# Kernel tuning notes

Hardware: AMD Instinct MI355X
Metric: run time of the kernel (lower is better)

## Reference

```python
import jax, jax.numpy as jnp
import numpy as np

HIDDEN = 2048
NUM_HEADS = 16
HEAD_DIM = 128
WINDOW = 256
BATCH = 2
SEQ = 2048
ROPE_BASE = 10000.0


def apply_rope(t):
    # t: [b, h, s, d]; half-split (rotate-half) rotary embedding
    d = t.shape[-1]
    s = t.shape[-2]
    inv_freq = 1.0 / (ROPE_BASE ** (jnp.arange(0, d, 2, dtype=jnp.float32) / d))  # [d/2]
    freqs = jnp.arange(s, dtype=jnp.float32)[:, None] * inv_freq[None, :]          # [s, d/2]
    cos, sin = jnp.cos(freqs), jnp.sin(freqs)
    t1, t2 = t[..., : d // 2], t[..., d // 2 :]
    return jnp.concatenate([t1 * cos - t2 * sin, t1 * sin + t2 * cos], axis=-1)


def setup_inputs() -> dict:
    key = jax.random.key(0)
    ks = jax.random.split(key, 10)
    dm = HEAD_DIM * NUM_HEADS
    lin_std = 1.0 / np.sqrt(HIDDEN)
    out_std = 1.0 / np.sqrt(dm)
    return {
        "x": jax.random.normal(ks[0], (BATCH, SEQ, HIDDEN), dtype=jnp.float32),
        "W_Q": jax.random.uniform(ks[1], (HIDDEN, dm), jnp.float32, -lin_std, lin_std),
        "b_Q": jax.random.uniform(ks[2], (dm,), jnp.float32, -lin_std, lin_std),
        "W_K": jax.random.uniform(ks[3], (HIDDEN, dm), jnp.float32, -lin_std, lin_std),
        "b_K": jax.random.uniform(ks[4], (dm,), jnp.float32, -lin_std, lin_std),
        "W_V": jax.random.uniform(ks[5], (HIDDEN, dm), jnp.float32, -lin_std, lin_std),
        "b_V": jax.random.uniform(ks[6], (dm,), jnp.float32, -lin_std, lin_std),
        "W_O": jax.random.uniform(ks[7], (dm, HIDDEN), jnp.float32, -out_std, out_std),
        "b_O": jax.random.uniform(ks[8], (HIDDEN,), jnp.float32, -out_std, out_std),
        "key_weights": jax.random.normal(ks[9], (NUM_HEADS,), dtype=jnp.float32),
    }


def reference(x, W_Q, b_Q, W_K, b_K, W_V, b_V, W_O, b_O, key_weights):
    b, s, _ = x.shape
    scale = HEAD_DIM ** -0.5

    def split_heads(t):  # [b, s, h*d] -> [b, h, s, d]
        return t.reshape(b, s, NUM_HEADS, HEAD_DIM).transpose(0, 2, 1, 3)

    q = split_heads(x @ W_Q + b_Q)
    k = split_heads(x @ W_K + b_K)
    v = split_heads(x @ W_V + b_V)

    q = apply_rope(q)
    k = apply_rope(k)

    # num_kv_heads == num_heads here, so group_size == 1: plain per-head attention
    scores = jnp.einsum("bhqd,bhkd->bhqk", q, k) * scale
    scores = scores * key_weights[None, :, None, None]

    # sliding-window causal mask: allow 0 <= i - j <= WINDOW
    i = jnp.arange(s)[:, None]
    j = jnp.arange(s)[None, :]
    allowed = (j <= i) & (j >= i - WINDOW)
    scores = jnp.where(allowed[None, None], scores, -jnp.inf)

    attn = jax.nn.softmax(scores, axis=-1)
    out = jnp.einsum("bhqk,bhkd->bhqd", attn, v)  # [b, h, s, d]
    out = out.transpose(0, 2, 1, 3).reshape(b, s, NUM_HEADS * HEAD_DIM)
    return out @ W_O + b_O
```

## Files before the change

### kernel.cpp

```cpp
#include <hip/hip_runtime.h>
#include <cstdint>

#define SEQn   2048
#define NHn    16
#define HDn    128
#define DMn    2048
#define HIDn   2048
#define BATCHn 2
#define WINn   256
#define MROWS  (BATCHn*SEQn)
#define WELEMS ((size_t)HIDn * DMn)

typedef short s16x8 __attribute__((ext_vector_type(8)));
typedef float f32x4 __attribute__((ext_vector_type(4)));

__device__ __forceinline__ float bf2f(ushort x) {
    union { uint u; float f; } v; v.u = ((uint)x) << 16; return v.f;
}
__device__ __forceinline__ ushort f2bf(float f) {
    union { float f; uint u; } v; v.f = f;
    uint u = v.u;
    return (ushort)((u + 0x7FFFu + ((u >> 16) & 1u)) >> 16);
}

#define GLOAD_LDS16(g, l) __builtin_amdgcn_global_load_lds(                   \
    (const __attribute__((address_space(1))) unsigned int*)(g),               \
    (__attribute__((address_space(3))) unsigned int*)(l), 16, 0, 0)

__global__ __launch_bounds__(256)
void transpose_all_kernel(const float* __restrict__ WQ, const float* __restrict__ WK,
                          const float* __restrict__ WV, const float* __restrict__ WO,
                          ushort* __restrict__ WT,
                          const float* __restrict__ x, ushort* __restrict__ xb)
{
    const int tid = threadIdx.y * 32 + threadIdx.x;
    if (blockIdx.z == 4) {
        const int bid = blockIdx.y * 64 + blockIdx.x;
        const size_t base = ((size_t)bid * 256 + tid) * 8;
        const float4 a0 = *reinterpret_cast<const float4*>(x + base);
        const float4 a1 = *reinterpret_cast<const float4*>(x + base + 4);
        ushort4 o0, o1;
        o0.x = f2bf(a0.x); o0.y = f2bf(a0.y); o0.z = f2bf(a0.z); o0.w = f2bf(a0.w);
        o1.x = f2bf(a1.x); o1.y = f2bf(a1.y); o1.z = f2bf(a1.z); o1.w = f2bf(a1.w);
        *reinterpret_cast<ushort4*>(xb + base)     = o0;
        *reinterpret_cast<ushort4*>(xb + base + 4) = o1;
        return;
    }
    __shared__ ushort t[32][33];
    const float* src = (blockIdx.z == 0) ? WQ : (blockIdx.z == 1) ? WK
                     : (blockIdx.z == 2) ? WV : WO;
    ushort* dst = WT + (size_t)blockIdx.z * WELEMS;
    const int tx = threadIdx.x, ty = threadIdx.y;
    const int n  = blockIdx.x * 32 + tx;
    const int k0 = blockIdx.y * 32;
    #pragma unroll
    for (int r = ty; r < 32; r += 8)
        t[r][tx] = f2bf(src[(size_t)(k0 + r) * 2048 + n]);
    __syncthreads();
    const int k  = k0 + tx;
    const int nb = blockIdx.x * 32;
    #pragma unroll
    for (int r = ty; r < 32; r += 8)
        dst[(size_t)(nb + r) * 2048 + k] = t[tx][r];
}

__global__ __launch_bounds__(256)
void transpose_cvt_kernel(const float* __restrict__ src, ushort* __restrict__ dst)
{
    __shared__ ushort t[32][33];
    const int tx = threadIdx.x, ty = threadIdx.y;
    const int n  = blockIdx.x * 32 + tx;
    const int k0 = blockIdx.y * 32;
    #pragma unroll
    for (int r = ty; r < 32; r += 8)
        t[r][tx] = f2bf(src[(size_t)(k0 + r) * 2048 + n]);
    __syncthreads();
    const int k  = k0 + tx;
    const int nb = blockIdx.x * 32;
    #pragma unroll
    for (int r = ty; r < 32; r += 8)
        dst[(size_t)(nb + r) * 2048 + k] = t[tx][r];
}

template<int ABF16>
__global__ __launch_bounds__(256)
void gemm_qkv_kernel(const void* __restrict__ Araw, const ushort* __restrict__ WT,
                     const float* __restrict__ bQ, const float* __restrict__ bK,
                     const float* __restrict__ bV,
                     ushort* __restrict__ Qb, ushort* __restrict__ Kb,
                     ushort* __restrict__ Vt)
{
    __shared__ __align__(16) ushort smem[128 * 136];
    ushort* As = smem;
    ushort* Bs = smem + 128 * 64;
    const int tid = threadIdx.x;
    const int m0  = blockIdx.y * 128;
    const int n0g = blockIdx.x * 128;
    const int sel = n0g >> 11;
    const int n0  = n0g & 2047;
    const ushort* BT  = WT + (size_t)sel * WELEMS;
    const float* bias = (sel == 0) ? bQ : (sel == 1) ? bK : bV;
    const int w  = tid >> 6;
    const int l  = tid & 63;
    const int wy = w >> 1, wx = w & 1;
    const int q  = l >> 4, lm = l & 15;
    const int sw = lm & 7;

    f32x4 acc[4][4];
    #pragma unroll
    for (int i = 0; i < 4; ++i)
        #pragma unroll
        for (int j = 0; j < 4; ++j) acc[i][j] = (f32x4)0.0f;

    for (int kt = 0; kt < HIDn; kt += 64) {
        if (ABF16) {
            #pragma unroll
            for (int it = 0; it < 4; ++it) {
                const int v = it * 256 + tid;
                const int r = v >> 3;
                const int cs = ((v & 7) ^ (r & 7)) << 3;
                const ushort* gA = (const ushort*)Araw + (size_t)(m0 + r) * HIDn + kt + cs;
                const ushort* gB = BT + (size_t)(n0 + r) * HIDn + kt + cs;
                GLOAD_LDS16(gA, As + (it * 256 + w * 64) * 8);
                GLOAD_LDS16(gB, Bs + (it * 256 + w * 64) * 8);
            }
        } else {
            #pragma unroll
            for (int it = 0; it < 4; ++it) {
                const int v = it * 256 + tid;
                const int r = v >> 3;
                const int c = (v & 7) << 3;
                const float* Af = (const float*)Araw + (size_t)(m0 + r) * HIDn + kt + c;
                const float4 a0 = *reinterpret_cast<const float4*>(Af);
                const float4 a1 = *reinterpret_cast<const float4*>(Af + 4);
                ushort* d = &As[(size_t)(v ^ (r & 7)) * 8];
                d[0] = f2bf(a0.x); d[1] = f2bf(a0.y); d[2] = f2bf(a0.z); d[3] = f2bf(a0.w);
                d[4] = f2bf(a1.x); d[5] = f2bf(a1.y); d[6] = f2bf(a1.z); d[7] = f2bf(a1.w);
                const int cs = ((v & 7) ^ (r & 7)) << 3;
                const ushort* gB = BT + (size_t)(n0 + r) * HIDn + kt + cs;
                GLOAD_LDS16(gB, Bs + (it * 256 + w * 64) * 8);
            }
        }
        __syncthreads();
        #pragma unroll
        for (int ks = 0; ks < 2; ++ks) {
            s16x8 af[4], bfv[4];
            #pragma unroll
            for (int im = 0; im < 4; ++im) {
                const int arow = wy * 64 + im * 16 + lm;
                af[im] = *reinterpret_cast<const s16x8*>(
                    &As[arow * 64 + (((ks * 4 + q) ^ sw) << 3)]);
            }
            #pragma unroll
            for (int in = 0; in < 4; ++in) {
                const int brow = wx * 64 + in * 16 + lm;
                bfv[in] = *reinterpret_cast<const s16x8*>(
                    &Bs[brow * 64 + (((ks * 4 + q) ^ sw) << 3)]);
            }
            #pragma unroll
            for (int im = 0; im < 4; ++im)
                #pragma unroll
                for (int in = 0; in < 4; ++in)
                    acc[im][in] = __builtin_amdgcn_mfma_f32_16x16x32_bf16(af[im], bfv[in], acc[im][in], 0, 0, 0);
        }
        __syncthreads();
    }

    if (sel == 2) {
        #pragma unroll
        for (int in = 0; in < 4; ++in) {
            const int gcol = n0 + wx * 64 + in * 16 + lm;
            const float bv = bias[gcol];
            #pragma unroll
            for (int im = 0; im < 4; ++im) {
                const int grow0 = m0 + wy * 64 + im * 16 + q * 4;
                #pragma unroll
                for (int r = 0; r < 4; ++r) {
                    const float val = acc[im][in][r] + bv;
                    const int grow = grow0 + r;
                    const int bb = grow >> 11, s = grow & (SEQn - 1);
                    const int hh = gcol >> 7,  d = gcol & (HDn - 1);
                    Vt[(((size_t)(bb * NHn + hh)) * HDn + d) * SEQn + s] = f2bf(val);
                }
            }
        }
    } else {
        ushort* ctile = smem;
        #pragma unroll
        for (int in = 0; in < 4; ++in) {
            const int col = wx * 64 + in * 16 + lm;
            const float bv = bias[n0 + col];
            #pragma unroll
            for (int im = 0; im < 4; ++im) {
                const int row0 = wy * 64 + im * 16 + q * 4;
                #pragma unroll
                for (int r = 0; r < 4; ++r)
                    ctile[(row0 + r) * 136 + col] = f2bf(acc[im][in][r] + bv);
            }
        }
        __syncthreads();
        ushort* dst = (sel == 0) ? Qb : Kb;
        const int d = tid & 63;
        const float invf = exp2f(-(float)d * 0.20762050593046f);
        for (int r = tid >> 6; r < 128; r += 4) {
            const int s = (m0 + r) & (SEQn - 1);
            const float ang = (float)s * invf;
            float sn, cs;
            __sincosf(ang, &sn, &cs);
            const float t1 = bf2f(ctile[r * 136 + d]);
            const float t2 = bf2f(ctile[r * 136 + 64 + d]);
            const size_t base = (size_t)(m0 + r) * DMn + n0 + d;
            dst[base]      = f2bf(t1 * cs - t2 * sn);
            dst[base + 64] = f2bf(t1 * sn + t2 * cs);
        }
    }
}

__global__ __launch_bounds__(256)
void gemm_out_kernel(const ushort* __restrict__ A, const ushort* __restrict__ BT,
                     const float* __restrict__ bias, float* __restrict__ C)
{
    __shared__ __align__(16) ushort As[64 * 64];
    __shared__ __align__(16) ushort Bs[128 * 64];
    const int tid = threadIdx.x;
    const int m0 = blockIdx.y * 64;
    const int n0 = blockIdx.x * 128;
    const int w  = tid >> 6;
    const int l  = tid & 63;
    const int wy = w >> 1, wx = w & 1;
    const int q  = l >> 4, lm = l & 15;
    const int sw = lm & 7;

    f32x4 acc[2][4];
    #pragma unroll
    for (int i = 0; i < 2; ++i)
        #pragma unroll
        for (int j = 0; j < 4; ++j) acc[i][j] = (f32x4)0.0f;

    for (int kt = 0; kt < DMn; kt += 64) {
        #pragma unroll
        for (int it = 0; it < 2; ++it) {
            const int v = it * 256 + tid;
            const int r = v >> 3;
            const int cs = ((v & 7) ^ (r & 7)) << 3;
            const ushort* gA = A + (size_t)(m0 + r) * DMn + kt + cs;
            GLOAD_LDS16(gA, As + (it * 256 + w * 64) * 8);
        }
        #pragma unroll
        for (int it = 0; it < 4; ++it) {
            const int v = it * 256 + tid;
            const int r = v >> 3;
            const int cs = ((v & 7) ^ (r & 7)) << 3;
            const ushort* gB = BT + (size_t)(n0 + r) * DMn + kt + cs;
            GLOAD_LDS16(gB, Bs + (it * 256 + w * 64) * 8);
        }
        __syncthreads();
        #pragma unroll
        for (int ks = 0; ks < 2; ++ks) {
            s16x8 af[2], bfv[4];
            #pragma unroll
            for (int im = 0; im < 2; ++im) {
                const int arow = wy * 32 + im * 16 + lm;
                af[im] = *reinterpret_cast<const s16x8*>(
                    &As[arow * 64 + (((ks * 4 + q) ^ sw) << 3)]);
            }
            #pragma unroll
            for (int in = 0; in < 4; ++in) {
                const int brow = wx * 64 + in * 16 + lm;
                bfv[in] = *reinterpret_cast<const s16x8*>(
                    &Bs[brow * 64 + (((ks * 4 + q) ^ sw) << 3)]);
            }
            #pragma unroll
            for (int im = 0; im < 2; ++im)
                #pragma unroll
                for (int in = 0; in < 4; ++in)
                    acc[im][in] = __builtin_amdgcn_mfma_f32_16x16x32_bf16(af[im], bfv[in], acc[im][in], 0, 0, 0);
        }
        __syncthreads();
    }
    #pragma unroll
    for (int in = 0; in < 4; ++in) {
        const int gcol = n0 + wx * 64 + in * 16 + lm;
        const float bv = bias[gcol];
        #pragma unroll
        for (int im = 0; im < 2; ++im) {
            const int grow0 = m0 + wy * 32 + im * 16 + q * 4;
            #pragma unroll
            for (int r = 0; r < 4; ++r)
                C[(size_t)(grow0 + r) * HIDn + gcol] = acc[im][in][r] + bv;
        }
    }
}

__global__ __launch_bounds__(256)
void attn_mfma_kernel(const ushort* Q, const ushort* __restrict__ K,
                      const ushort* __restrict__ Vt, const float* __restrict__ kw,
                      ushort* AO)
{
    __shared__ ushort plds[4][16 * 40];
    const int w  = threadIdx.x >> 6;
    const int l  = threadIdx.x & 63;
    const int q  = l >> 4, lm = l & 15;
    const int gw = blockIdx.x * 4 + w;
    const int qt = gw & 127;
    const int h  = (gw >> 7) & (NHn - 1);
    const int b  = gw >> 11;
    const int q0 = qt * 16;
    const float f = kw[h] * 0.08838834764831845f;

    s16x8 qf[4];
    const size_t qbase = ((size_t)(b * SEQn + q0 + lm)) * DMn + h * HDn;
    #pragma unroll
    for (int ks = 0; ks < 4; ++ks)
        qf[ks] = *reinterpret_cast<const s16x8*>(Q + qbase + ks * 32 + q * 8);

    f32x4 O[8];
    #pragma unroll
    for (int nt = 0; nt < 8; ++nt) O[nt] = (f32x4)0.0f;
    float m[4]    = {-1e30f, -1e30f, -1e30f, -1e30f};
    float lsum[4] = {0.f, 0.f, 0.f, 0.f};

    const int lo = q0 - WINn;
    const int c0 = lo > 0 ? (lo & ~31) : 0;
    const int nch = (q0 + 16 - c0 + 31) >> 5;

    const size_t kbh = ((size_t)(b * SEQn)) * DMn + h * HDn;
    const size_t vbh = ((size_t)(b * NHn + h)) * HDn * SEQn;

    for (int c = 0; c < nch; ++c) {
        const int kc = c0 + c * 32;
        s16x8 vf[8];
        #pragma unroll
        for (int nt = 0; nt < 8; ++nt)
            vf[nt] = *reinterpret_cast<const s16x8*>(
                Vt + vbh + (size_t)(nt * 16 + lm) * SEQn + kc + q * 8);
        f32x4 S[2];
        #pragma unroll
        for (int t = 0; t < 2; ++t) {
            f32x4 acc = (f32x4)0.0f;
            const size_t krow = kbh + (size_t)(kc + t * 16 + lm) * DMn;
            #pragma unroll
            for (int ks = 0; ks < 4; ++ks) {
                const s16x8 kf = *reinterpret_cast<const s16x8*>(K + krow + ks * 32 + q * 8);
                acc = __builtin_amdgcn_mfma_f32_16x16x32_bf16(qf[ks], kf, acc, 0, 0, 0);
            }
            S[t] = acc;
        }
        const int j0 = kc + lm, j1 = kc + 16 + lm;
        #pragma unroll
        for (int r = 0; r < 4; ++r) {
            const int i = q0 + q * 4 + r;
            float v0 = S[0][r] * f;
            float v1 = S[1][r] * f;
            if (j0 > i || j0 < i - WINn) v0 = -1e30f;
            if (j1 > i || j1 < i - WINn) v1 = -1e30f;
            float mx = fmaxf(v0, v1);
            #pragma unroll
            for (int off = 8; off > 0; off >>= 1)
                mx = fmaxf(mx, __shfl_xor(mx, off));
            const float mn = fmaxf(m[r], mx);
            const float alpha = __expf(m[r] - mn);
            m[r] = mn;
            const ushort h0 = f2bf(__expf(v0 - mn));
            const ushort h1 = f2bf(__expf(v1 - mn));
            plds[w][(q * 4 + r) * 40 + lm]      = h0;
            plds[w][(q * 4 + r) * 40 + 16 + lm] = h1;
            float ps = bf2f(h0) + bf2f(h1);
            #pragma unroll
            for (int off = 8; off > 0; off >>= 1)
                ps += __shfl_xor(ps, off);
            lsum[r] = lsum[r] * alpha + ps;
            #pragma unroll
            for (int nt = 0; nt < 8; ++nt) O[nt][r] *= alpha;
        }
        const s16x8 pf = *reinterpret_cast<const s16x8*>(&plds[w][lm * 40 + q * 8]);
        #pragma unroll
        for (int nt = 0; nt < 8; ++nt)
            O[nt] = __builtin_amdgcn_mfma_f32_16x16x32_bf16(pf, vf[nt], O[nt], 0, 0, 0);
    }
    #pragma unroll
    for (int r = 0; r < 4; ++r) {
        const float inv = 1.0f / lsum[r];
        const size_t orow = ((size_t)(b * SEQn + q0 + q * 4 + r)) * DMn + h * HDn;
        #pragma unroll
        for (int nt = 0; nt < 8; ++nt)
            AO[orow + nt * 16 + lm] = f2bf(O[nt][r] * inv);
    }
}

extern "C" void kernel_launch(void* const* d_in, const int* in_sizes, int n_in,
                              void* d_out, int out_size, void* d_ws, size_t ws_size,
                              hipStream_t stream)
{
    (void)in_sizes; (void)n_in; (void)out_size;
    const float* x  = (const float*)d_in[0];
    const float* WQ = (const float*)d_in[1];
    const float* bQ = (const float*)d_in[2];
    const float* WK = (const float*)d_in[3];
    const float* bK = (const float*)d_in[4];
    const float* WV = (const float*)d_in[5];
    const float* bV = (const float*)d_in[6];
    const float* WO = (const float*)d_in[7];
    const float* bO = (const float*)d_in[8];
    const float* kw = (const float*)d_in[9];
    float* out = (float*)d_out;

    char* ws = (char*)d_ws;
    const size_t AELEMS = (size_t)MROWS * DMn;
    ushort* Qb = (ushort*)ws;
    ushort* Kb = (ushort*)(ws + AELEMS * 2);
    ushort* Vt = (ushort*)(ws + AELEMS * 4);
    ushort* WT = (ushort*)(ws + AELEMS * 6);
    const size_t FULL = AELEMS * 6 + WELEMS * 8 + AELEMS * 2;
    const bool have_full = ws_size >= FULL;
    ushort* xb = (ushort*)(ws + AELEMS * 6 + WELEMS * 8);

    const dim3 tblk(32, 8);

    if (have_full) {
        transpose_all_kernel<<<dim3(64, 64, 5), tblk, 0, stream>>>(WQ, WK, WV, WO, WT, x, xb);
        gemm_qkv_kernel<1><<<dim3(3 * DMn / 128, MROWS / 128), 256, 0, stream>>>(
            xb, WT, bQ, bK, bV, Qb, Kb, Vt);
        attn_mfma_kernel<<<dim3(BATCHn * NHn * (SEQn / 16) / 4), 256, 0, stream>>>(Qb, Kb, Vt, kw, Qb);
        gemm_out_kernel<<<dim3(HIDn / 128, MROWS / 64), 256, 0, stream>>>(
            Qb, WT + 3 * WELEMS, bO, out);
    } else {
        transpose_all_kernel<<<dim3(64, 64, 3), tblk, 0, stream>>>(WQ, WK, WV, WO, WT, x, xb);
        gemm_qkv_kernel<0><<<dim3(3 * DMn / 128, MROWS / 128), 256, 0, stream>>>(
            x, WT, bQ, bK, bV, Qb, Kb, Vt);
        attn_mfma_kernel<<<dim3(BATCHn * NHn * (SEQn / 16) / 4), 256, 0, stream>>>(Qb, Kb, Vt, kw, Qb);
        transpose_cvt_kernel<<<dim3(64, 64), tblk, 0, stream>>>(WO, WT);
        gemm_out_kernel<<<dim3(HIDn / 128, MROWS / 64), 256, 0, stream>>>(Qb, WT, bO, out);
    }
}
```

Measured before the change: 403.6 us.

## Double-buffer GEMM LDS tiles, stage V transpose via LDS, add MFMA priority hints

Both GEMM kernels now use two LDS slots. The next K-tile's global-to-LDS loads are issued before computing the current tile, with explicit vmcnt waits and raw barriers, so memory latency can overlap MFMA work. The V projection epilogue writes its transposed tile to LDS first and then stores it coalesced to Vt, replacing scattered 2-byte stores. s_setprio raises wave priority around the MFMA blocks in the GEMMs and attention, and the attention K fragments are loaded before their MFMAs. The doubled LDS footprint may lower occupancy, and the hand-written waitcnt counts must match the number of loads issued per stage.

New measurement: 374.5 us. 7.2% less time.

```diff
diff --git a/kernel.cpp b/kernel.cpp
--- a/kernel.cpp
+++ b/kernel.cpp
@@ -26,6 +26,9 @@
 #define GLOAD_LDS16(g, l) __builtin_amdgcn_global_load_lds(                   \
     (const __attribute__((address_space(1))) unsigned int*)(g),               \
     (__attribute__((address_space(3))) unsigned int*)(l), 16, 0, 0)
+
+#define FENCE() do { asm volatile("" ::: "memory");                           \
+                     __builtin_amdgcn_sched_barrier(0); } while (0)
 
 __global__ __launch_bounds__(256)
 void transpose_all_kernel(const float* __restrict__ WQ, const float* __restrict__ WK,
@@ -90,9 +93,7 @@
                      ushort* __restrict__ Qb, ushort* __restrict__ Kb,
                      ushort* __restrict__ Vt)
 {
-    __shared__ __align__(16) ushort smem[128 * 136];
-    ushort* As = smem;
-    ushort* Bs = smem + 128 * 64;
+    __shared__ __align__(16) ushort smem[32768];
     const int tid = threadIdx.x;
     const int m0  = blockIdx.y * 128;
     const int n0g = blockIdx.x * 128;
@@ -112,7 +113,9 @@
         #pragma unroll
         for (int j = 0; j < 4; ++j) acc[i][j] = (f32x4)0.0f;
 
-    for (int kt = 0; kt < HIDn; kt += 64) {
+    auto stage = [&](int slot, int kt) {
+        ushort* AsS = smem + slot * 16384;
+        ushort* BsS = AsS + 8192;
         if (ABF16) {
             #pragma unroll
             for (int it = 0; it < 4; ++it) {
@@ -121,8 +124,8 @@
                 const int cs = ((v & 7) ^ (r & 7)) << 3;
                 const ushort* gA = (const ushort*)Araw + (size_t)(m0 + r) * HIDn + kt + cs;
                 const ushort* gB = BT + (size_t)(n0 + r) * HIDn + kt + cs;
-                GLOAD_LDS16(gA, As + (it * 256 + w * 64) * 8);
-                GLOAD_LDS16(gB, Bs + (it * 256 + w * 64) * 8);
+                GLOAD_LDS16(gA, AsS + (it * 256 + w * 64) * 8);
+                GLOAD_LDS16(gB, BsS + (it * 256 + w * 64) * 8);
             }
         } else {
             #pragma unroll
@@ -133,15 +136,19 @@
                 const float* Af = (const float*)Araw + (size_t)(m0 + r) * HIDn + kt + c;
                 const float4 a0 = *reinterpret_cast<const float4*>(Af);
                 const float4 a1 = *reinterpret_cast<const float4*>(Af + 4);
-                ushort* d = &As[(size_t)(v ^ (r & 7)) * 8];
+                ushort* d = &AsS[(size_t)(v ^ (r & 7)) * 8];
                 d[0] = f2bf(a0.x); d[1] = f2bf(a0.y); d[2] = f2bf(a0.z); d[3] = f2bf(a0.w);
                 d[4] = f2bf(a1.x); d[5] = f2bf(a1.y); d[6] = f2bf(a1.z); d[7] = f2bf(a1.w);
                 const int cs = ((v & 7) ^ (r & 7)) << 3;
                 const ushort* gB = BT + (size_t)(n0 + r) * HIDn + kt + cs;
-                GLOAD_LDS16(gB, Bs + (it * 256 + w * 64) * 8);
-            }
-        }
-        __syncthreads();
+                GLOAD_LDS16(gB, BsS + (it * 256 + w * 64) * 8);
+            }
+        }
+    };
+
+    auto compute = [&](int slot) {
+        const ushort* AsS = smem + slot * 16384;
+        const ushort* BsS = AsS + 8192;
         #pragma unroll
         for (int ks = 0; ks < 2; ++ks) {
             s16x8 af[4], bfv[4];
@@ -149,40 +156,74 @@
             for (int im = 0; im < 4; ++im) {
                 const int arow = wy * 64 + im * 16 + lm;
                 af[im] = *reinterpret_cast<const s16x8*>(
-                    &As[arow * 64 + (((ks * 4 + q) ^ sw) << 3)]);
+                    &AsS[arow * 64 + (((ks * 4 + q) ^ sw) << 3)]);
             }
             #pragma unroll
             for (int in = 0; in < 4; ++in) {
                 const int brow = wx * 64 + in * 16 + lm;
                 bfv[in] = *reinterpret_cast<const s16x8*>(
-                    &Bs[brow * 64 + (((ks * 4 + q) ^ sw) << 3)]);
-            }
+                    &BsS[brow * 64 + (((ks * 4 + q) ^ sw) << 3)]);
+            }
+            __builtin_amdgcn_s_setprio(1);
             #pragma unroll
             for (int im = 0; im < 4; ++im)
                 #pragma unroll
                 for (int in = 0; in < 4; ++in)
                     acc[im][in] = __builtin_amdgcn_mfma_f32_16x16x32_bf16(af[im], bfv[in], acc[im][in], 0, 0, 0);
+            __builtin_amdgcn_s_setprio(0);
+        }
+    };
+
+    const int NT = HIDn / 64;
+    stage(0, 0);
+    int cur = 0;
+    for (int t = 0; t < NT - 1; ++t) {
+        stage(cur ^ 1, (t + 1) * 64);
+        if (ABF16) asm volatile("s_waitcnt vmcnt(8)" ::: "memory");
+        else       asm volatile("s_waitcnt vmcnt(4)" ::: "memory");
+        __builtin_amdgcn_s_barrier();
+        FENCE();
+        compute(cur);
+        FENCE();
+        if (!ABF16) asm volatile("s_waitcnt lgkmcnt(0)" ::: "memory");
+        __builtin_amdgcn_s_barrier();
+        FENCE();
+        cur ^= 1;
+    }
+    asm volatile("s_waitcnt vmcnt(0)" ::: "memory");
+    __builtin_amdgcn_s_barrier();
+    FENCE();
+    compute(cur);
+    __syncthreads();
+
+    if (sel == 2) {
+        ushort* ctile = smem;
+        #pragma unroll
+        for (int in = 0; in < 4; ++in) {
+            const int col = wx * 64 + in * 16 + lm;
+            const float bv = bias[n0 + col];
+            #pragma unroll
+            for (int im = 0; im < 4; ++im) {
+                const int row0 = wy * 64 + im * 16 + q * 4;
+                #pragma unroll
+                for (int r = 0; r < 4; ++r)
+                    ctile[col * 136 + row0 + r] = f2bf(acc[im][in][r] + bv);
+            }
         }
         __syncthreads();
-    }
-
-    if (sel == 2) {
-        #pragma unroll
-        for (int in = 0; in < 4; ++in) {
-            const int gcol = n0 + wx * 64 + in * 16 + lm;
-            const float bv = bias[gcol];
-            #pragma unroll
-            for (int im = 0; im < 4; ++im) {
-                const int grow0 = m0 + wy * 64 + im * 16 + q * 4;
-                #pragma unroll
-                for (int r = 0; r < 4; ++r) {
-                    const float val = acc[im][in][r] + bv;
-                    const int grow = grow0 + r;
-                    const int bb = grow >> 11, s = grow & (SEQn - 1);
-                    const int hh = gcol >> 7,  d = gcol & (HDn - 1);
-                    Vt[(((size_t)(bb * NHn + hh)) * HDn + d) * SEQn + s] = f2bf(val);
-                }
-            }
+        const int hh = n0 >> 7;
+        const int bb = m0 >> 11;
+        const int s0 = m0 & (SEQn - 1);
+        const int st = (tid & 15) * 8;
+        const int d0 = tid >> 4;
+        #pragma unroll
+        for (int db = 0; db < 8; ++db) {
+            const int d = d0 + db * 16;
+            const ushort4 v0 = *reinterpret_cast<const ushort4*>(&ctile[d * 136 + st]);
+            const ushort4 v1 = *reinterpret_cast<const ushort4*>(&ctile[d * 136 + st + 4]);
+            ushort* dstp = Vt + (((size_t)(bb * NHn + hh)) * HDn + d) * SEQn + s0 + st;
+            *reinterpret_cast<ushort4*>(dstp)     = v0;
+            *reinterpret_cast<ushort4*>(dstp + 4) = v1;
         }
     } else {
         ushort* ctile = smem;
@@ -220,8 +261,7 @@
 void gemm_out_kernel(const ushort* __restrict__ A, const ushort* __restrict__ BT,
                      const float* __restrict__ bias, float* __restrict__ C)
 {
-    __shared__ __align__(16) ushort As[64 * 64];
-    __shared__ __align__(16) ushort Bs[128 * 64];
+    __shared__ __align__(16) ushort smem[24576];
     const int tid = threadIdx.x;
     const int m0 = blockIdx.y * 64;
     const int n0 = blockIdx.x * 128;
@@ -237,24 +277,30 @@
         #pragma unroll
         for (int j = 0; j < 4; ++j) acc[i][j] = (f32x4)0.0f;
 
-    for (int kt = 0; kt < DMn; kt += 64) {
+    auto stage = [&](int slot, int kt) {
+        ushort* AsS = smem + slot * 12288;
+        ushort* BsS = AsS + 4096;
         #pragma unroll
         for (int it = 0; it < 2; ++it) {
             const int v = it * 256 + tid;
             const int r = v >> 3;
             const int cs = ((v & 7) ^ (r & 7)) << 3;
-            const ushort* gA = A + (size_t)(m0 + r) * DMn + kt + cs;
-            GLOAD_LDS16(gA, As + (it * 256 + w * 64) * 8);
+            GLOAD_LDS16(A + (size_t)(m0 + r) * DMn + kt + cs,
+                        AsS + (it * 256 + w * 64) * 8);
         }
         #pragma unroll
         for (int it = 0; it < 4; ++it) {
             const int v = it * 256 + tid;
             const int r = v >> 3;
             const int cs = ((v & 7) ^ (r & 7)) << 3;
-            const ushort* gB = BT + (size_t)(n0 + r) * DMn + kt + cs;
-            GLOAD_LDS16(gB, Bs + (it * 256 + w * 64) * 8);
-        }
-        __syncthreads();
+            GLOAD_LDS16(BT + (size_t)(n0 + r) * DMn + kt + cs,
+                        BsS + (it * 256 + w * 64) * 8);
+        }
+    };
+
+    auto compute = [&](int slot) {
+        const ushort* AsS = smem + slot * 12288;
+        const ushort* BsS = AsS + 4096;
         #pragma unroll
         for (int ks = 0; ks < 2; ++ks) {
             s16x8 af[2], bfv[4];
@@ -262,22 +308,43 @@
             for (int im = 0; im < 2; ++im) {
                 const int arow = wy * 32 + im * 16 + lm;
                 af[im] = *reinterpret_cast<const s16x8*>(
-                    &As[arow * 64 + (((ks * 4 + q) ^ sw) << 3)]);
+                    &AsS[arow * 64 + (((ks * 4 + q) ^ sw) << 3)]);
             }
             #pragma unroll
             for (int in = 0; in < 4; ++in) {
                 const int brow = wx * 64 + in * 16 + lm;
                 bfv[in] = *reinterpret_cast<const s16x8*>(
-                    &Bs[brow * 64 + (((ks * 4 + q) ^ sw) << 3)]);
-            }
+                    &BsS[brow * 64 + (((ks * 4 + q) ^ sw) << 3)]);
+            }
+            __builtin_amdgcn_s_setprio(1);
             #pragma unroll
             for (int im = 0; im < 2; ++im)
                 #pragma unroll
                 for (int in = 0; in < 4; ++in)
                     acc[im][in] = __builtin_amdgcn_mfma_f32_16x16x32_bf16(af[im], bfv[in], acc[im][in], 0, 0, 0);
-        }
-        __syncthreads();
-    }
+            __builtin_amdgcn_s_setprio(0);
+        }
+    };
+
+    const int NT = DMn / 64;
+    stage(0, 0);
+    int cur = 0;
+    for (int t = 0; t < NT - 1; ++t) {
+        stage(cur ^ 1, (t + 1) * 64);
+        asm volatile("s_waitcnt vmcnt(6)" ::: "memory");
+        __builtin_amdgcn_s_barrier();
+        FENCE();
+        compute(cur);
+        FENCE();
+        __builtin_amdgcn_s_barrier();
+        FENCE();
+        cur ^= 1;
+    }
+    asm volatile("s_waitcnt vmcnt(0)" ::: "memory");
+    __builtin_amdgcn_s_barrier();
+    FENCE();
+    compute(cur);
+
     #pragma unroll
     for (int in = 0; in < 4; ++in) {
         const int gcol = n0 + wx * 64 + in * 16 + lm;
@@ -339,11 +406,15 @@
         for (int t = 0; t < 2; ++t) {
             f32x4 acc = (f32x4)0.0f;
             const size_t krow = kbh + (size_t)(kc + t * 16 + lm) * DMn;
-            #pragma unroll
-            for (int ks = 0; ks < 4; ++ks) {
-                const s16x8 kf = *reinterpret_cast<const s16x8*>(K + krow + ks * 32 + q * 8);
-                acc = __builtin_amdgcn_mfma_f32_16x16x32_bf16(qf[ks], kf, acc, 0, 0, 0);
-            }
+            s16x8 kf[4];
+            #pragma unroll
+            for (int ks = 0; ks < 4; ++ks)
+                kf[ks] = *reinterpret_cast<const s16x8*>(K + krow + ks * 32 + q * 8);
+            __builtin_amdgcn_s_setprio(1);
+            #pragma unroll
+            for (int ks = 0; ks < 4; ++ks)
+                acc = __builtin_amdgcn_mfma_f32_16x16x32_bf16(qf[ks], kf[ks], acc, 0, 0, 0);
+            __builtin_amdgcn_s_setprio(0);
             S[t] = acc;
         }
         const int j0 = kc + lm, j1 = kc + 16 + lm;
@@ -374,9 +445,11 @@
             for (int nt = 0; nt < 8; ++nt) O[nt][r] *= alpha;
         }
         const s16x8 pf = *reinterpret_cast<const s16x8*>(&plds[w][lm * 40 + q * 8]);
+        __builtin_amdgcn_s_setprio(1);
         #pragma unroll
         for (int nt = 0; nt < 8; ++nt)
             O[nt] = __builtin_amdgcn_mfma_f32_16x16x32_bf16(pf, vf[nt], O[nt], 0, 0, 0);
+        __builtin_amdgcn_s_setprio(0);
     }
     #pragma unroll
     for (int r = 0; r < 4; ++r) {
```
